# Optimization experiments

Measured on AMD Instinct MI355X. Metric: run time of the kernel, lower is better.

Reference implementation:

```python
import jax, jax.numpy as jnp
import numpy as np

NEG_SLOPE = 0.2  # PyG GATConv default leaky_relu slope


def gat_conv(h_in, src, dst, W, a_src, a_dst, b, N):
    # h_in: [N, Fin]; src/dst: [E] (self-loops already appended)
    h = h_in @ W                      # [N, Fout]
    alpha_src = h @ a_src             # [N]
    alpha_dst = h @ a_dst             # [N]
    e = jax.nn.leaky_relu(alpha_src[src] + alpha_dst[dst], NEG_SLOPE)  # [E]
    # segment softmax over incoming edges of each destination node
    m = jax.ops.segment_max(e, dst, num_segments=N)
    m = jnp.where(jnp.isfinite(m), m, 0.0)
    p = jnp.exp(e - m[dst])
    denom = jax.ops.segment_sum(p, dst, num_segments=N)
    alpha = p / jnp.maximum(denom[dst], 1e-16)
    out = jax.ops.segment_sum(alpha[:, None] * h[src], dst, num_segments=N)
    return out + b


def setup_inputs() -> dict:
    key = jax.random.key(0)
    ks = jax.random.split(key, 16)
    N, E, V, D, H, C, G = 100000, 1600000, 128, 50, 16, 10, 512
    x = jax.random.normal(ks[0], (N, V), dtype=jnp.float32)
    edge_index = jax.random.randint(ks[1], (2, E), 0, N, dtype=jnp.int32)
    batch = jnp.sort(jax.random.randint(ks[2], (N,), 0, G, dtype=jnp.int32))
    s = lambda fan: 1.0 / np.sqrt(fan)
    return {
        "x": x, "edge_index": edge_index, "batch": batch,
        "embedding": jax.random.normal(ks[3], (V, D), dtype=jnp.float32),
        "W1": jax.random.normal(ks[4], (D, H), dtype=jnp.float32) * s(D),
        "a_src1": jax.random.normal(ks[5], (H,), dtype=jnp.float32) * s(H),
        "a_dst1": jax.random.normal(ks[6], (H,), dtype=jnp.float32) * s(H),
        "b1": jnp.zeros((H,), dtype=jnp.float32),
        "W2": jax.random.normal(ks[7], (H, H), dtype=jnp.float32) * s(H),
        "a_src2": jax.random.normal(ks[8], (H,), dtype=jnp.float32) * s(H),
        "a_dst2": jax.random.normal(ks[9], (H,), dtype=jnp.float32) * s(H),
        "b2": jnp.zeros((H,), dtype=jnp.float32),
        "W3": jax.random.normal(ks[10], (H, C), dtype=jnp.float32) * s(H),
        "a_src3": jax.random.normal(ks[11], (C,), dtype=jnp.float32) * s(C),
        "a_dst3": jax.random.normal(ks[12], (C,), dtype=jnp.float32) * s(C),
        "b3": jnp.zeros((C,), dtype=jnp.float32),
    }


def reference(x, edge_index, batch, embedding, W1, a_src1, a_dst1, b1,
              W2, a_src2, a_dst2, b2, W3, a_src3, a_dst3, b3):
    N = x.shape[0]
    G = 512  # num graphs
    # embedding lookup via argmax over one-hot-ish features
    idx = jnp.argmax(x, axis=1)
    h = embedding[idx]                               # [N, 50]
    # add self-loops once (PyG GATConv default)
    loops = jnp.arange(N, dtype=edge_index.dtype)
    src = jnp.concatenate([edge_index[0], loops])
    dst = jnp.concatenate([edge_index[1], loops])
    h = jax.nn.relu(gat_conv(h, src, dst, W1, a_src1, a_dst1, b1, N))
    # dropout: eval mode -> identity
    h = jax.nn.relu(gat_conv(h, src, dst, W2, a_src2, a_dst2, b2, N))
    h = gat_conv(h, src, dst, W3, a_src3, a_dst3, b3, N)  # [N, C]
    # global mean pool over graphs
    sums = jax.ops.segment_sum(h, batch, num_segments=G)
    cnts = jax.ops.segment_sum(jnp.ones((N,), h.dtype), batch, num_segments=G)
    pooled = sums / jnp.maximum(cnts, 1.0)[:, None]
    return jax.nn.softmax(pooled, axis=1)
```

## Files before the change

### kernel.cpp

```cpp
#include <hip/hip_runtime.h>
#include <math.h>

#define NEG_SLOPE 0.2f
#define NBUK_MAX 512

typedef float v4f __attribute__((ext_vector_type(4)));
typedef _Float16 h4v __attribute__((ext_vector_type(4)));

template <int B2>
__global__ void __launch_bounds__(1024)
k_histarg(const float* __restrict__ x, const int* __restrict__ edst, int E,
          int* __restrict__ histT, int NBUK, int* __restrict__ idx, int N, int V) {
    __shared__ int sh[NBUK_MAX];
    int t = threadIdx.x;
    if ((int)blockIdx.x < B2) {
        int b = blockIdx.x;
        for (int k = t; k < NBUK; k += 1024) sh[k] = 0;
        __syncthreads();
        long long ebeg = (long long)b * E / B2, eend = (long long)(b + 1) * E / B2;
        for (long long i = ebeg + t; i < eend; i += 1024)
            atomicAdd(&sh[edst[i] >> 8], 1);
        __syncthreads();
        for (int k = t; k < NBUK; k += 1024) histT[(long long)k * B2 + b] = sh[k];
    } else {
        int node = ((int)blockIdx.x - B2) * 32 + (t >> 5);
        int lane = t & 31;
        if (node >= N) return;
        const v4f* row = (const v4f*)(x + (long long)node * V);
        float bv = -INFINITY;
        int bi = 0x7fffffff;
        int nq = V >> 2;
        for (int q = lane; q < nq; q += 32) {
            v4f v = row[q];
            int base = q << 2;
            if (v.x > bv || (v.x == bv && base     < bi)) { bv = v.x; bi = base;     }
            if (v.y > bv || (v.y == bv && base + 1 < bi)) { bv = v.y; bi = base + 1; }
            if (v.z > bv || (v.z == bv && base + 2 < bi)) { bv = v.z; bi = base + 2; }
            if (v.w > bv || (v.w == bv && base + 3 < bi)) { bv = v.w; bi = base + 3; }
        }
        for (int off = 16; off > 0; off >>= 1) {
            float ov = __shfl_down(bv, off, 32);
            int   oi = __shfl_down(bi, off, 32);
            if (ov > bv || (ov == bv && oi < bi)) { bv = ov; bi = oi; }
        }
        if (lane == 0) idx[node] = bi;
    }
}

template <int FIN, int FOUT>
__global__ void __launch_bounds__(256)
k_scan_tr(const int* __restrict__ vals, int* __restrict__ excl, int* __restrict__ bsums, int M,
          const float* __restrict__ emb, const int* __restrict__ idx,
          const float* __restrict__ W, const float* __restrict__ a_src,
          const float* __restrict__ a_dst, _Float16* __restrict__ h_t,
          float* __restrict__ asrc, float* __restrict__ adst, int N, int NB_SCAN) {
    __shared__ int s[256];
    __shared__ float sW[FIN * FOUT];
    __shared__ float sa[FOUT], sd[FOUT];
    int t = threadIdx.x;
    if ((int)blockIdx.x < NB_SCAN) {
        int i = blockIdx.x * 256 + t;
        int v = (i < M) ? vals[i] : 0;
        s[t] = v;
        __syncthreads();
        for (int off = 1; off < 256; off <<= 1) {
            int a = (t >= off) ? s[t - off] : 0;
            __syncthreads();
            s[t] += a;
            __syncthreads();
        }
        if (i < M) excl[i] = s[t] - v;
        if (t == 255) bsums[blockIdx.x] = s[255];
    } else {
        for (int i = t; i < FIN * FOUT; i += 256) sW[i] = W[i];
        if (t < FOUT) { sa[t] = a_src[t]; sd[t] = a_dst[t]; }
        __syncthreads();
        int n = ((int)blockIdx.x - NB_SCAN) * 256 + t;
        if (n >= N) return;
        float acc[FOUT];
#pragma unroll
        for (int f = 0; f < FOUT; f++) acc[f] = 0.f;
        const float* hr = emb + (long long)idx[n] * FIN;
        for (int k = 0; k < FIN; k++) {
            float v = hr[k];
#pragma unroll
            for (int f = 0; f < FOUT; f++) acc[f] += v * sW[k * FOUT + f];
        }
        float s1 = 0.f, s2 = 0.f;
        _Float16 hh[16];
#pragma unroll
        for (int f = 0; f < 16; f++) hh[f] = (_Float16)0.f;
#pragma unroll
        for (int f = 0; f < FOUT; f++) {
            hh[f] = (_Float16)acc[f];
            s1 += acc[f] * sa[f];
            s2 += acc[f] * sd[f];
        }
        uint4* dst = (uint4*)(h_t + (long long)n * 16);
        dst[0] = ((uint4*)hh)[0];
        dst[1] = ((uint4*)hh)[1];
        asrc[n] = s1;
        adst[n] = s2;
    }
}

template <int B2>
__global__ void __launch_bounds__(1024)
k_scatB(const int* __restrict__ esrc, const int* __restrict__ edst, int E,
        const int* __restrict__ sexcl, const int* __restrict__ bsums,
        int* __restrict__ tmp, int NBUK) {
    __shared__ int cur[NBUK_MAX];
    __shared__ int bex[512];
    int t = threadIdx.x, b = blockIdx.x;
    if (t < 512) bex[t] = (t < NBUK) ? bsums[t] : 0;
    __syncthreads();
    for (int off = 1; off < 512; off <<= 1) {
        int a = (t < 512 && t >= off) ? bex[t - off] : 0;
        __syncthreads();
        if (t < 512) bex[t] += a;
        __syncthreads();
    }
    for (int k = t; k < NBUK; k += 1024)
        cur[k] = sexcl[(long long)k * B2 + b] + (k ? bex[k - 1] : 0);
    __syncthreads();
    long long ebeg = (long long)b * E / B2, eend = (long long)(b + 1) * E / B2;
    for (long long i = ebeg + t; i < eend; i += 1024) {
        int d = edst[i];
        int pos = atomicAdd(&cur[d >> 8], 1);
        tmp[pos] = ((d & 255) << 17) | esrc[i];
    }
}

template <int B2>
__global__ void __launch_bounds__(256)
k_binB(const int* __restrict__ sexcl, const int* __restrict__ bsums,
       const int* __restrict__ tmp,
       int* __restrict__ rowptr, int* __restrict__ csr_src, int N, int NBUK, int E) {
    __shared__ int bx[512];
    __shared__ int cnt[256];
    __shared__ int scn[256];
    __shared__ int cur[256];
    int t = threadIdx.x, b = blockIdx.x;
    bx[t]       = (t < NBUK)       ? bsums[t]       : 0;
    bx[t + 256] = (t + 256 < NBUK) ? bsums[t + 256] : 0;
    __syncthreads();
    for (int off = 1; off < 512; off <<= 1) {
        int a0 = (t >= off) ? bx[t - off] : 0;
        int a1 = (t + 256 >= off) ? bx[t + 256 - off] : 0;
        __syncthreads();
        bx[t] += a0;
        bx[t + 256] += a1;
        __syncthreads();
    }
    int t0 = sexcl[(long long)b * B2] + (b ? bx[b - 1] : 0);
    int t1 = (b + 1 < NBUK) ? (sexcl[(long long)(b + 1) * B2] + bx[b]) : E;
    cnt[t] = 0;
    __syncthreads();
    for (int i = t0 + t; i < t1; i += 256) atomicAdd(&cnt[tmp[i] >> 17], 1);
    __syncthreads();
    int v = cnt[t];
    scn[t] = v;
    __syncthreads();
    for (int off = 1; off < 256; off <<= 1) {
        int a = (t >= off) ? scn[t - off] : 0;
        __syncthreads();
        scn[t] += a;
        __syncthreads();
    }
    int base = t0 + scn[t] - v;
    int d = (b << 8) + t;
    if (d < N) rowptr[d] = base;
    cur[t] = base;
    if (d == N - 1) rowptr[N] = E;
    __syncthreads();
    for (int i = t0 + t; i < t1; i += 256) {
        int p = tmp[i];
        int pos = atomicAdd(&cur[p >> 17], 1);
        csr_src[pos] = p & 0x1FFFF;
    }
}

template <typename EPI>
__device__ __forceinline__ void gat_core4(const int* __restrict__ rowptr,
                                          const int* __restrict__ csr_src,
                                          const float* __restrict__ asrc,
                                          const float* __restrict__ adst,
                                          const _Float16* __restrict__ h_t,
                                          int d, int l4, EPI epilogue) {
    const h4v* __restrict__ H = (const h4v*)h_t;
    int r0 = rowptr[d], r1 = rowptr[d + 1];
    float ad = adst[d];

    float e0 = asrc[d] + ad;
    e0 = (e0 >= 0.f) ? e0 : NEG_SLOPE * e0;
    float p0 = __expf(e0);
    h4v hd = H[(long long)d * 4 + l4];
    float a0 = p0 * (float)hd[0], a1 = p0 * (float)hd[1];
    float a2 = p0 * (float)hd[2], a3 = p0 * (float)hd[3];
    float psum = (l4 == 0) ? p0 : 0.f;

    int rem = r1 - r0;
    if (rem > 0) {
        int j = r0;
        int s = (l4 < rem) ? csr_src[j + l4] : d;
        float av = asrc[s];
        while (true) {
            int remn = rem - 4;
            int s2 = d; float av2 = 0.f;
            if (remn > 0) {
                s2 = (l4 < remn) ? csr_src[j + 4 + l4] : d;
                av2 = asrc[s2];
            }
            float e = av + ad;
            e = (e >= 0.f) ? e : NEG_SLOPE * e;
            float p = (l4 < rem) ? __expf(e) : 0.f;
            psum += p;
#pragma unroll
            for (int k = 0; k < 4; k++) {
                float pk = __shfl(p, k, 4);
                int   sk = __shfl(s, k, 4);
                h4v hh = H[(long long)sk * 4 + l4];
                a0 += pk * (float)hh[0];
                a1 += pk * (float)hh[1];
                a2 += pk * (float)hh[2];
                a3 += pk * (float)hh[3];
            }
            if (remn <= 0) break;
            j += 4; rem = remn; s = s2; av = av2;
        }
    }
    psum += __shfl_xor(psum, 1, 4);
    psum += __shfl_xor(psum, 2, 4);
    float inv = 1.f / fmaxf(psum, 1e-16f);
    epilogue(d, a0 * inv, a1 * inv, a2 * inv, a3 * inv);
}

template <int FN>
__global__ void __launch_bounds__(256)
k_gat_ft(const int* __restrict__ rowptr, const int* __restrict__ csr_src,
         const float* __restrict__ asrc, const float* __restrict__ adst,
         const _Float16* __restrict__ h_t, const float* __restrict__ bias,
         const float* __restrict__ Wn, const float* __restrict__ an_src,
         const float* __restrict__ an_dst,
         _Float16* __restrict__ h_next, float* __restrict__ asrc_n,
         float* __restrict__ adst_n, int N) {
    __shared__ float sW[16 * 16];
    __shared__ float sa[16], sd[16], sb[16];
    int t = threadIdx.x;
    {
        int k = t >> 4, f = t & 15;
        sW[t] = (f < FN) ? Wn[k * FN + f] : 0.f;
    }
    if (t < 16) {
        sa[t] = (t < FN) ? an_src[t] : 0.f;
        sd[t] = (t < FN) ? an_dst[t] : 0.f;
        sb[t] = bias[t];
    }
    __syncthreads();

    int gid = blockIdx.x * 256 + t;
    int d = gid >> 2, l4 = gid & 3;
    if (d >= N) return;

    gat_core4(rowptr, csr_src, asrc, adst, h_t, d, l4,
        [&](int dd, float v0, float v1, float v2, float v3) {
            int f0 = l4 * 4;
            float vv[4];
            vv[0] = fmaxf(v0 + sb[f0    ], 0.f);
            vv[1] = fmaxf(v1 + sb[f0 + 1], 0.f);
            vv[2] = fmaxf(v2 + sb[f0 + 2], 0.f);
            vv[3] = fmaxf(v3 + sb[f0 + 3], 0.f);
            float o0 = 0.f, o1 = 0.f, o2 = 0.f, o3 = 0.f;
#pragma unroll
            for (int q = 0; q < 4; q++) {
#pragma unroll
                for (int i = 0; i < 4; i++) {
                    float vk = __shfl(vv[i], q, 4);
                    const float* wr = &sW[(q * 4 + i) * 16 + f0];
                    o0 += vk * wr[0];
                    o1 += vk * wr[1];
                    o2 += vk * wr[2];
                    o3 += vk * wr[3];
                }
            }
            float c1 = o0 * sa[f0] + o1 * sa[f0 + 1] + o2 * sa[f0 + 2] + o3 * sa[f0 + 3];
            float c2 = o0 * sd[f0] + o1 * sd[f0 + 1] + o2 * sd[f0 + 2] + o3 * sd[f0 + 3];
            c1 += __shfl_xor(c1, 1, 4); c1 += __shfl_xor(c1, 2, 4);
            c2 += __shfl_xor(c2, 1, 4); c2 += __shfl_xor(c2, 2, 4);
            h4v ho = { (_Float16)o0, (_Float16)o1, (_Float16)o2, (_Float16)o3 };
            ((h4v*)h_next)[(long long)dd * 4 + l4] = ho;
            if (l4 == 0) { asrc_n[dd] = c1; adst_n[dd] = c2; }
        });
}

__global__ void __launch_bounds__(256)
k_gat_last(const int* __restrict__ rowptr, const int* __restrict__ csr_src,
           const float* __restrict__ asrc, const float* __restrict__ adst,
           const _Float16* __restrict__ h_t, float* __restrict__ out, int N) {
    int gid = blockIdx.x * 256 + threadIdx.x;
    int d = gid >> 2, l4 = gid & 3;
    if (d >= N) return;
    gat_core4(rowptr, csr_src, asrc, adst, h_t, d, l4,
        [&](int dd, float v0, float v1, float v2, float v3) {
            v4f o = { v0, v1, v2, v3 };
            ((v4f*)out)[(long long)dd * 4 + l4] = o;
        });
}

__global__ void k_pool(const float* __restrict__ h3, const int* __restrict__ batch,
                       const float* __restrict__ b3, float* __restrict__ out, int N, int C) {
    int g = blockIdx.x;
    int lo = 0, hi = N;
    while (lo < hi) { int mid = (lo + hi) >> 1; if (batch[mid] < g) lo = mid + 1; else hi = mid; }
    int start = lo;
    hi = N;
    while (lo < hi) { int mid = (lo + hi) >> 1; if (batch[mid] < g + 1) lo = mid + 1; else hi = mid; }
    int end = lo;

    float sum[16];
    for (int f = 0; f < C; f++) sum[f] = 0.f;
    for (int n = start + threadIdx.x; n < end; n += blockDim.x) {
        const float* r = h3 + (long long)n * 16;
        for (int f = 0; f < C; f++) sum[f] += r[f];
    }
    __shared__ float red[256 * 16];
    for (int f = 0; f < C; f++) red[threadIdx.x * 16 + f] = sum[f];
    __syncthreads();
    for (int str = blockDim.x / 2; str > 0; str >>= 1) {
        if ((int)threadIdx.x < str)
            for (int f = 0; f < C; f++) red[threadIdx.x * 16 + f] += red[(threadIdx.x + str) * 16 + f];
        __syncthreads();
    }
    if (threadIdx.x == 0) {
        float cnt = fmaxf((float)(end - start), 1.f);
        float vals[16];
        float mx = -INFINITY;
        for (int f = 0; f < C; f++) { vals[f] = red[f] / cnt + b3[f]; mx = fmaxf(mx, vals[f]); }
        float se = 0.f;
        for (int f = 0; f < C; f++) { vals[f] = __expf(vals[f] - mx); se += vals[f]; }
        for (int f = 0; f < C; f++) out[(long long)g * C + f] = vals[f] / se;
    }
}

extern "C" void kernel_launch(void* const* d_in, const int* in_sizes, int n_in,
                              void* d_out, int out_size, void* d_ws, size_t ws_size,
                              hipStream_t stream) {
    const float* x    = (const float*)d_in[0];
    const int*   eidx = (const int*)d_in[1];
    const int*   batch= (const int*)d_in[2];
    const float* emb  = (const float*)d_in[3];
    const float* W1   = (const float*)d_in[4];
    const float* as1  = (const float*)d_in[5];
    const float* ad1  = (const float*)d_in[6];
    const float* b1   = (const float*)d_in[7];
    const float* W2   = (const float*)d_in[8];
    const float* as2  = (const float*)d_in[9];
    const float* ad2  = (const float*)d_in[10];
    const float* b2   = (const float*)d_in[11];
    const float* W3   = (const float*)d_in[12];
    const float* as3  = (const float*)d_in[13];
    const float* ad3  = (const float*)d_in[14];
    const float* b3   = (const float*)d_in[15];

    const int H = in_sizes[5];
    const int C = in_sizes[13];
    const int D = in_sizes[4] / H;
    const int V = in_sizes[3] / D;
    const int N = in_sizes[0] / V;
    const int E = in_sizes[1] / 2;
    const int G = out_size / C;
    const int* esrc = eidx;
    const int* edst = eidx + E;
    const int NBUK = (N + 255) >> 8;
    constexpr int B2 = 256;
    const int M = NBUK * B2;

    char* w = (char*)d_ws;
    auto carve = [&](size_t bytes) {
        char* p = w;
        w += (bytes + 255) & ~(size_t)255;
        return p;
    };
    float*     as_a    = (float*)carve((size_t)N * 4);
    float*     ad_a    = (float*)carve((size_t)N * 4);
    float*     as_b    = (float*)carve((size_t)N * 4);
    float*     ad_b    = (float*)carve((size_t)N * 4);
    int*       idx     = (int*)carve((size_t)N * 4);
    int*       rowptr  = (int*)carve((size_t)(N + 1) * 4);
    int*       csr_src = (int*)carve((size_t)E * 4);
    int*       histT   = (int*)carve((size_t)M * 4);
    int*       sexcl   = (int*)carve((size_t)M * 4);
    int*       bsums   = (int*)carve(2048 * 4);
    _Float16*  hTa     = (_Float16*)carve((size_t)N * 16 * 2);
    _Float16*  hTb     = (_Float16*)carve((size_t)N * 16 * 2);
    size_t zone_bytes = ((size_t)E * 4 > (size_t)N * 64) ? (size_t)E * 4 : (size_t)N * 64;
    char*  zone = carve(zone_bytes);
    float* X0  = (float*)zone;
    int*   tmp = (int*)zone;
    (void)ws_size; (void)n_in;

    const int BT = 256;
    dim3 blk(BT);
    int gGat4 = (N * 4 + BT - 1) / BT;
    int nb2   = (M + 255) / 256;
    int gArg  = (N + 31) / 32;
    int gTr   = (N + BT - 1) / BT;

    k_histarg<B2><<<B2 + gArg, dim3(1024), 0, stream>>>(x, edst, E, histT, NBUK, idx, N, V);

    k_scan_tr<50, 16><<<nb2 + gTr, blk, 0, stream>>>(histT, sexcl, bsums, M,
                                                     emb, idx, W1, as1, ad1, hTa, as_a, ad_a, N, nb2);

    k_scatB<B2><<<B2, dim3(1024), 0, stream>>>(esrc, edst, E, sexcl, bsums, tmp, NBUK);
    k_binB<B2><<<NBUK, blk, 0, stream>>>(sexcl, bsums, tmp, rowptr, csr_src, N, NBUK, E);

    k_gat_ft<16><<<gGat4, blk, 0, stream>>>(rowptr, csr_src, as_a, ad_a, hTa, b1,
                                            W2, as2, ad2, hTb, as_b, ad_b, N);

    k_gat_ft<10><<<gGat4, blk, 0, stream>>>(rowptr, csr_src, as_b, ad_b, hTb, b2,
                                            W3, as3, ad3, hTa, as_a, ad_a, N);

    k_gat_last<<<gGat4, blk, 0, stream>>>(rowptr, csr_src, as_a, ad_a, hTa, X0, N);

    k_pool<<<G, blk, 0, stream>>>(X0, batch, b3, (float*)d_out, N, C);
}
```

Baseline: 254.6 us.

## Build CSR via global-degree atomics, pack node records, process nodes degree-sorted

Measured after the change: 456.7 us. 79.4% more time.

```diff
diff --git a/kernel.cpp b/kernel.cpp
--- a/kernel.cpp
+++ b/kernel.cpp
@@ -2,26 +2,22 @@
 #include <math.h>
 
 #define NEG_SLOPE 0.2f
-#define NBUK_MAX 512
 
 typedef float v4f __attribute__((ext_vector_type(4)));
 typedef _Float16 h4v __attribute__((ext_vector_type(4)));
+
+#define RECB 64
 
 template <int B2>
 __global__ void __launch_bounds__(1024)
 k_histarg(const float* __restrict__ x, const int* __restrict__ edst, int E,
-          int* __restrict__ histT, int NBUK, int* __restrict__ idx, int N, int V) {
-    __shared__ int sh[NBUK_MAX];
+          int* __restrict__ deg, int* __restrict__ idx, int N, int V) {
     int t = threadIdx.x;
     if ((int)blockIdx.x < B2) {
         int b = blockIdx.x;
-        for (int k = t; k < NBUK; k += 1024) sh[k] = 0;
-        __syncthreads();
         long long ebeg = (long long)b * E / B2, eend = (long long)(b + 1) * E / B2;
         for (long long i = ebeg + t; i < eend; i += 1024)
-            atomicAdd(&sh[edst[i] >> 8], 1);
-        __syncthreads();
-        for (int k = t; k < NBUK; k += 1024) histT[(long long)k * B2 + b] = sh[k];
+            atomicAdd(&deg[edst[i]], 1);
     } else {
         int node = ((int)blockIdx.x - B2) * 32 + (t >> 5);
         int lane = t & 31;
@@ -49,33 +45,29 @@
 
 template <int FIN, int FOUT>
 __global__ void __launch_bounds__(256)
-k_scan_tr(const int* __restrict__ vals, int* __restrict__ excl, int* __restrict__ bsums, int M,
-          const float* __restrict__ emb, const int* __restrict__ idx,
-          const float* __restrict__ W, const float* __restrict__ a_src,
-          const float* __restrict__ a_dst, _Float16* __restrict__ h_t,
-          float* __restrict__ asrc, float* __restrict__ adst, int N, int NB_SCAN) {
-    __shared__ int s[256];
+k_sum_tr(const int* __restrict__ deg, int* __restrict__ bsums, int M,
+         const float* __restrict__ emb, const int* __restrict__ idx,
+         const float* __restrict__ W, const float* __restrict__ a_src,
+         const float* __restrict__ a_dst, char* __restrict__ rec,
+         int N, int NB_SUM) {
     __shared__ float sW[FIN * FOUT];
     __shared__ float sa[FOUT], sd[FOUT];
+    __shared__ int s[256];
     int t = threadIdx.x;
-    if ((int)blockIdx.x < NB_SCAN) {
+    if ((int)blockIdx.x < NB_SUM) {
         int i = blockIdx.x * 256 + t;
-        int v = (i < M) ? vals[i] : 0;
-        s[t] = v;
-        __syncthreads();
-        for (int off = 1; off < 256; off <<= 1) {
-            int a = (t >= off) ? s[t - off] : 0;
+        s[t] = (i < M) ? deg[i] : 0;
+        __syncthreads();
+        for (int str = 128; str > 0; str >>= 1) {
+            if (t < str) s[t] += s[t + str];
             __syncthreads();
-            s[t] += a;
-            __syncthreads();
-        }
-        if (i < M) excl[i] = s[t] - v;
-        if (t == 255) bsums[blockIdx.x] = s[255];
+        }
+        if (t == 0) bsums[blockIdx.x] = s[0];
     } else {
         for (int i = t; i < FIN * FOUT; i += 256) sW[i] = W[i];
         if (t < FOUT) { sa[t] = a_src[t]; sd[t] = a_dst[t]; }
         __syncthreads();
-        int n = ((int)blockIdx.x - NB_SCAN) * 256 + t;
+        int n = ((int)blockIdx.x - NB_SUM) * 256 + t;
         if (n >= N) return;
         float acc[FOUT];
 #pragma unroll
@@ -96,50 +88,23 @@
             s1 += acc[f] * sa[f];
             s2 += acc[f] * sd[f];
         }
-        uint4* dst = (uint4*)(h_t + (long long)n * 16);
-        dst[0] = ((uint4*)hh)[0];
-        dst[1] = ((uint4*)hh)[1];
-        asrc[n] = s1;
-        adst[n] = s2;
-    }
-}
-
-template <int B2>
-__global__ void __launch_bounds__(1024)
-k_scatB(const int* __restrict__ esrc, const int* __restrict__ edst, int E,
-        const int* __restrict__ sexcl, const int* __restrict__ bsums,
-        int* __restrict__ tmp, int NBUK) {
-    __shared__ int cur[NBUK_MAX];
-    __shared__ int bex[512];
-    int t = threadIdx.x, b = blockIdx.x;
-    if (t < 512) bex[t] = (t < NBUK) ? bsums[t] : 0;
-    __syncthreads();
-    for (int off = 1; off < 512; off <<= 1) {
-        int a = (t < 512 && t >= off) ? bex[t - off] : 0;
-        __syncthreads();
-        if (t < 512) bex[t] += a;
-        __syncthreads();
-    }
-    for (int k = t; k < NBUK; k += 1024)
-        cur[k] = sexcl[(long long)k * B2 + b] + (k ? bex[k - 1] : 0);
-    __syncthreads();
-    long long ebeg = (long long)b * E / B2, eend = (long long)(b + 1) * E / B2;
-    for (long long i = ebeg + t; i < eend; i += 1024) {
-        int d = edst[i];
-        int pos = atomicAdd(&cur[d >> 8], 1);
-        tmp[pos] = ((d & 255) << 17) | esrc[i];
-    }
-}
-
-template <int B2>
+        char* r = rec + (long long)n * RECB;
+        *(uint4*)(r)      = ((uint4*)hh)[0];
+        *(uint4*)(r + 16) = ((uint4*)hh)[1];
+        float2 am; am.x = s1; am.y = s2;
+        *(float2*)(r + 32) = am;
+    }
+}
+
 __global__ void __launch_bounds__(256)
-k_binB(const int* __restrict__ sexcl, const int* __restrict__ bsums,
-       const int* __restrict__ tmp,
-       int* __restrict__ rowptr, int* __restrict__ csr_src, int N, int NBUK, int E) {
+k_rowptr(const int* __restrict__ deg, const int* __restrict__ bsums,
+         int* __restrict__ cur, int* __restrict__ perm, char* __restrict__ recA,
+         int N, int NBUK) {
     __shared__ int bx[512];
-    __shared__ int cnt[256];
-    __shared__ int scn[256];
-    __shared__ int cur[256];
+    __shared__ int h1[256];
+    __shared__ int h2[256];
+    __shared__ int sdv[256];
+    __shared__ int ssc[256];
     int t = threadIdx.x, b = blockIdx.x;
     bx[t]       = (t < NBUK)       ? bsums[t]       : 0;
     bx[t + 256] = (t + 256 < NBUK) ? bsums[t + 256] : 0;
@@ -152,49 +117,82 @@
         bx[t + 256] += a1;
         __syncthreads();
     }
-    int t0 = sexcl[(long long)b * B2] + (b ? bx[b - 1] : 0);
-    int t1 = (b + 1 < NBUK) ? (sexcl[(long long)(b + 1) * B2] + bx[b]) : E;
-    cnt[t] = 0;
-    __syncthreads();
-    for (int i = t0 + t; i < t1; i += 256) atomicAdd(&cnt[tmp[i] >> 17], 1);
-    __syncthreads();
-    int v = cnt[t];
-    scn[t] = v;
+    int chunk = b ? bx[b - 1] : 0;
+    int d = b * 256 + t;
+    bool valid = d < N;
+    int dg = valid ? deg[d] : 0;
+
+    h1[t] = 0;
+    __syncthreads();
+    int key = 255 - min(dg, 255);
+    if (valid) atomicAdd(&h1[key], 1);
+    __syncthreads();
+    int v = h1[t];
+    h2[t] = v;
     __syncthreads();
     for (int off = 1; off < 256; off <<= 1) {
-        int a = (t >= off) ? scn[t - off] : 0;
-        __syncthreads();
-        scn[t] += a;
-        __syncthreads();
-    }
-    int base = t0 + scn[t] - v;
-    int d = (b << 8) + t;
-    if (d < N) rowptr[d] = base;
-    cur[t] = base;
-    if (d == N - 1) rowptr[N] = E;
-    __syncthreads();
-    for (int i = t0 + t; i < t1; i += 256) {
-        int p = tmp[i];
-        int pos = atomicAdd(&cur[p >> 17], 1);
-        csr_src[pos] = p & 0x1FFFF;
+        int a = (t >= off) ? h2[t - off] : 0;
+        __syncthreads();
+        h2[t] += a;
+        __syncthreads();
+    }
+    h1[t] = h2[t] - v;
+    __syncthreads();
+    int r = 0;
+    if (valid) r = atomicAdd(&h1[key], 1);
+
+    sdv[t] = 0;
+    __syncthreads();
+    if (valid) sdv[r] = dg;
+    __syncthreads();
+    int sv = sdv[t];
+    ssc[t] = sv;
+    __syncthreads();
+    for (int off = 1; off < 256; off <<= 1) {
+        int a = (t >= off) ? ssc[t - off] : 0;
+        __syncthreads();
+        ssc[t] += a;
+        __syncthreads();
+    }
+    if (valid) {
+        int r0 = chunk + ssc[r] - dg;
+        cur[d] = r0;
+        int2 m; m.x = r0; m.y = r0 + dg;
+        *(int2*)(recA + (long long)d * RECB + 40) = m;
+        perm[b * 256 + r] = d;
+    }
+}
+
+__global__ void __launch_bounds__(256)
+k_scat(const int* __restrict__ esrc, const int* __restrict__ edst, int E,
+       int* __restrict__ cur, int* __restrict__ csr) {
+    int i = (blockIdx.x * 256 + threadIdx.x) * 4;
+    if (i + 4 <= E) {
+        int4 s4 = *(const int4*)(esrc + i);
+        int4 d4 = *(const int4*)(edst + i);
+        int p0 = atomicAdd(&cur[d4.x], 1); csr[p0] = s4.x;
+        int p1 = atomicAdd(&cur[d4.y], 1); csr[p1] = s4.y;
+        int p2 = atomicAdd(&cur[d4.z], 1); csr[p2] = s4.z;
+        int p3 = atomicAdd(&cur[d4.w], 1); csr[p3] = s4.w;
+    } else if (i < E) {
+        for (; i < E; i++) { int p = atomicAdd(&cur[edst[i]], 1); csr[p] = esrc[i]; }
     }
 }
 
 template <typename EPI>
-__device__ __forceinline__ void gat_core4(const int* __restrict__ rowptr,
+__device__ __forceinline__ void gat_core4(const char* __restrict__ rec,
                                           const int* __restrict__ csr_src,
-                                          const float* __restrict__ asrc,
-                                          const float* __restrict__ adst,
-                                          const _Float16* __restrict__ h_t,
                                           int d, int l4, EPI epilogue) {
-    const h4v* __restrict__ H = (const h4v*)h_t;
-    int r0 = rowptr[d], r1 = rowptr[d + 1];
-    float ad = adst[d];
-
-    float e0 = asrc[d] + ad;
+    const char* rd = rec + (long long)d * RECB;
+    int4 meta = *(const int4*)(rd + 32);
+    float as_d = __int_as_float(meta.x);
+    float ad   = __int_as_float(meta.y);
+    int r0 = meta.z, r1 = meta.w;
+
+    float e0 = as_d + ad;
     e0 = (e0 >= 0.f) ? e0 : NEG_SLOPE * e0;
     float p0 = __expf(e0);
-    h4v hd = H[(long long)d * 4 + l4];
+    h4v hd = *(const h4v*)(rd + l4 * 8);
     float a0 = p0 * (float)hd[0], a1 = p0 * (float)hd[1];
     float a2 = p0 * (float)hd[2], a3 = p0 * (float)hd[3];
     float psum = (l4 == 0) ? p0 : 0.f;
@@ -203,13 +201,13 @@
     if (rem > 0) {
         int j = r0;
         int s = (l4 < rem) ? csr_src[j + l4] : d;
-        float av = asrc[s];
+        float av = *(const float*)(rec + (long long)s * RECB + 32);
         while (true) {
             int remn = rem - 4;
             int s2 = d; float av2 = 0.f;
             if (remn > 0) {
                 s2 = (l4 < remn) ? csr_src[j + 4 + l4] : d;
-                av2 = asrc[s2];
+                av2 = *(const float*)(rec + (long long)s2 * RECB + 32);
             }
             float e = av + ad;
             e = (e >= 0.f) ? e : NEG_SLOPE * e;
@@ -219,7 +217,7 @@
             for (int k = 0; k < 4; k++) {
                 float pk = __shfl(p, k, 4);
                 int   sk = __shfl(s, k, 4);
-                h4v hh = H[(long long)sk * 4 + l4];
+                h4v hh = *(const h4v*)(rec + (long long)sk * RECB + l4 * 8);
                 a0 += pk * (float)hh[0];
                 a1 += pk * (float)hh[1];
                 a2 += pk * (float)hh[2];
@@ -232,18 +230,15 @@
     psum += __shfl_xor(psum, 1, 4);
     psum += __shfl_xor(psum, 2, 4);
     float inv = 1.f / fmaxf(psum, 1e-16f);
-    epilogue(d, a0 * inv, a1 * inv, a2 * inv, a3 * inv);
+    epilogue(d, r0, r1, a0 * inv, a1 * inv, a2 * inv, a3 * inv);
 }
 
 template <int FN>
 __global__ void __launch_bounds__(256)
-k_gat_ft(const int* __restrict__ rowptr, const int* __restrict__ csr_src,
-         const float* __restrict__ asrc, const float* __restrict__ adst,
-         const _Float16* __restrict__ h_t, const float* __restrict__ bias,
+k_gat_ft(const char* __restrict__ rec, const int* __restrict__ csr_src,
+         const int* __restrict__ perm, const float* __restrict__ bias,
          const float* __restrict__ Wn, const float* __restrict__ an_src,
-         const float* __restrict__ an_dst,
-         _Float16* __restrict__ h_next, float* __restrict__ asrc_n,
-         float* __restrict__ adst_n, int N) {
+         const float* __restrict__ an_dst, char* __restrict__ rec_next, int N) {
     __shared__ float sW[16 * 16];
     __shared__ float sa[16], sd[16], sb[16];
     int t = threadIdx.x;
@@ -259,11 +254,12 @@
     __syncthreads();
 
     int gid = blockIdx.x * 256 + t;
-    int d = gid >> 2, l4 = gid & 3;
-    if (d >= N) return;
-
-    gat_core4(rowptr, csr_src, asrc, adst, h_t, d, l4,
-        [&](int dd, float v0, float v1, float v2, float v3) {
+    int grp = gid >> 2, l4 = gid & 3;
+    if (grp >= N) return;
+    int d = perm[grp];
+
+    gat_core4(rec, csr_src, d, l4,
+        [&](int dd, int r0, int r1, float v0, float v1, float v2, float v3) {
             int f0 = l4 * 4;
             float vv[4];
             vv[0] = fmaxf(v0 + sb[f0    ], 0.f);
@@ -287,21 +283,27 @@
             float c2 = o0 * sd[f0] + o1 * sd[f0 + 1] + o2 * sd[f0 + 2] + o3 * sd[f0 + 3];
             c1 += __shfl_xor(c1, 1, 4); c1 += __shfl_xor(c1, 2, 4);
             c2 += __shfl_xor(c2, 1, 4); c2 += __shfl_xor(c2, 2, 4);
+            char* rn = rec_next + (long long)dd * RECB;
             h4v ho = { (_Float16)o0, (_Float16)o1, (_Float16)o2, (_Float16)o3 };
-            ((h4v*)h_next)[(long long)dd * 4 + l4] = ho;
-            if (l4 == 0) { asrc_n[dd] = c1; adst_n[dd] = c2; }
+            *(h4v*)(rn + l4 * 8) = ho;
+            if (l4 == 0) {
+                int4 m;
+                m.x = __float_as_int(c1); m.y = __float_as_int(c2);
+                m.z = r0; m.w = r1;
+                *(int4*)(rn + 32) = m;
+            }
         });
 }
 
 __global__ void __launch_bounds__(256)
-k_gat_last(const int* __restrict__ rowptr, const int* __restrict__ csr_src,
-           const float* __restrict__ asrc, const float* __restrict__ adst,
-           const _Float16* __restrict__ h_t, float* __restrict__ out, int N) {
+k_gat_last(const char* __restrict__ rec, const int* __restrict__ csr_src,
+           const int* __restrict__ perm, float* __restrict__ out, int N) {
     int gid = blockIdx.x * 256 + threadIdx.x;
-    int d = gid >> 2, l4 = gid & 3;
-    if (d >= N) return;
-    gat_core4(rowptr, csr_src, asrc, adst, h_t, d, l4,
-        [&](int dd, float v0, float v1, float v2, float v3) {
+    int grp = gid >> 2, l4 = gid & 3;
+    if (grp >= N) return;
+    int d = perm[grp];
+    gat_core4(rec, csr_src, d, l4,
+        [&](int dd, int r0, int r1, float v0, float v1, float v2, float v3) {
             v4f o = { v0, v1, v2, v3 };
             ((v4f*)out)[(long long)dd * 4 + l4] = o;
         });
@@ -371,9 +373,8 @@
     const int G = out_size / C;
     const int* esrc = eidx;
     const int* edst = eidx + E;
-    const int NBUK = (N + 255) >> 8;
     constexpr int B2 = 256;
-    const int M = NBUK * B2;
+    const int nb2 = (N + 255) / 256;
 
     char* w = (char*)d_ws;
     auto carve = [&](size_t bytes) {
@@ -381,46 +382,39 @@
         w += (bytes + 255) & ~(size_t)255;
         return p;
     };
-    float*     as_a    = (float*)carve((size_t)N * 4);
-    float*     ad_a    = (float*)carve((size_t)N * 4);
-    float*     as_b    = (float*)carve((size_t)N * 4);
-    float*     ad_b    = (float*)carve((size_t)N * 4);
-    int*       idx     = (int*)carve((size_t)N * 4);
-    int*       rowptr  = (int*)carve((size_t)(N + 1) * 4);
-    int*       csr_src = (int*)carve((size_t)E * 4);
-    int*       histT   = (int*)carve((size_t)M * 4);
-    int*       sexcl   = (int*)carve((size_t)M * 4);
-    int*       bsums   = (int*)carve(2048 * 4);
-    _Float16*  hTa     = (_Float16*)carve((size_t)N * 16 * 2);
-    _Float16*  hTb     = (_Float16*)carve((size_t)N * 16 * 2);
-    size_t zone_bytes = ((size_t)E * 4 > (size_t)N * 64) ? (size_t)E * 4 : (size_t)N * 64;
-    char*  zone = carve(zone_bytes);
-    float* X0  = (float*)zone;
-    int*   tmp = (int*)zone;
+    int*   idx     = (int*)carve((size_t)N * 4);
+    int*   deg     = (int*)carve((size_t)N * 4);
+    int*   cur     = (int*)carve((size_t)N * 4);
+    int*   perm    = (int*)carve((size_t)N * 4);
+    int*   bsums   = (int*)carve(2048 * 4);
+    int*   csr_src = (int*)carve((size_t)E * 4);
+    char*  recA    = carve((size_t)N * RECB);
+    char*  recB    = carve((size_t)N * RECB);
+    float* X0      = (float*)carve((size_t)N * 64);
     (void)ws_size; (void)n_in;
 
     const int BT = 256;
     dim3 blk(BT);
     int gGat4 = (N * 4 + BT - 1) / BT;
-    int nb2   = (M + 255) / 256;
     int gArg  = (N + 31) / 32;
     int gTr   = (N + BT - 1) / BT;
-
-    k_histarg<B2><<<B2 + gArg, dim3(1024), 0, stream>>>(x, edst, E, histT, NBUK, idx, N, V);
-
-    k_scan_tr<50, 16><<<nb2 + gTr, blk, 0, stream>>>(histT, sexcl, bsums, M,
-                                                     emb, idx, W1, as1, ad1, hTa, as_a, ad_a, N, nb2);
-
-    k_scatB<B2><<<B2, dim3(1024), 0, stream>>>(esrc, edst, E, sexcl, bsums, tmp, NBUK);
-    k_binB<B2><<<NBUK, blk, 0, stream>>>(sexcl, bsums, tmp, rowptr, csr_src, N, NBUK, E);
-
-    k_gat_ft<16><<<gGat4, blk, 0, stream>>>(rowptr, csr_src, as_a, ad_a, hTa, b1,
-                                            W2, as2, ad2, hTb, as_b, ad_b, N);
-
-    k_gat_ft<10><<<gGat4, blk, 0, stream>>>(rowptr, csr_src, as_b, ad_b, hTb, b2,
-                                            W3, as3, ad3, hTa, as_a, ad_a, N);
-
-    k_gat_last<<<gGat4, blk, 0, stream>>>(rowptr, csr_src, as_a, ad_a, hTa, X0, N);
+    int gScat = (E / 4 + BT - 1) / BT;
+
+    hipMemsetAsync(deg, 0, (size_t)N * 4, stream);
+
+    k_histarg<B2><<<B2 + gArg, dim3(1024), 0, stream>>>(x, edst, E, deg, idx, N, V);
+
+    k_sum_tr<50, 16><<<nb2 + gTr, blk, 0, stream>>>(deg, bsums, N,
+                                                    emb, idx, W1, as1, ad1, recA, N, nb2);
+
+    k_rowptr<<<nb2, blk, 0, stream>>>(deg, bsums, cur, perm, recA, N, nb2);
+    k_scat<<<gScat, blk, 0, stream>>>(esrc, edst, E, cur, csr_src);
+
+    k_gat_ft<16><<<gGat4, blk, 0, stream>>>(recA, csr_src, perm, b1, W2, as2, ad2, recB, N);
+
+    k_gat_ft<10><<<gGat4, blk, 0, stream>>>(recB, csr_src, perm, b2, W3, as3, ad3, recA, N);
+
+    k_gat_last<<<gGat4, blk, 0, stream>>>(recA, csr_src, perm, X0, N);
 
     k_pool<<<G, blk, 0, stream>>>(X0, batch, b3, (float*)d_out, N, C);
 }
```
